# Kernel optimization log

Measured on AMD Instinct MI355X. Metric: run time of the kernel, lower is better.

The kernel has to match this reference:

```python
import jax, jax.numpy as jnp
import numpy as np

P_SCALAR = 40.0
NEG_INF = -1e9


def setup_inputs() -> dict:
    key = jax.random.key(0)
    ks = jax.random.split(key, 6)
    B, Dk, Dv, T, H, W = 2, 128, 512, 2, 64, 64
    qkey = jax.random.normal(ks[0], (B, Dk, H, W), dtype=jnp.float32)
    qval = jax.random.normal(ks[1], (B, Dv, H, W), dtype=jnp.float32)
    mkey = jax.random.normal(ks[2], (B, Dk, T, H, W), dtype=jnp.float32)
    mval = jax.random.normal(ks[3], (B, Dv, T, H, W), dtype=jnp.float32)
    qmask = jax.random.bernoulli(ks[4], 0.5, (B, 1, H, W))
    mmask = jax.random.bernoulli(ks[5], 0.5, (B, 1, T, H, W))
    return {"qkey": qkey, "qval": qval, "qmask": qmask,
            "mkey": mkey, "mval": mval, "mmask": mmask}


def reference(qkey, qval, qmask, mkey, mval, mmask):
    # Faithful vectorized version of maskRead: for each batch, attention from
    # masked query pixels over masked memory pixels, scatter back into zeros.
    # Boolean-gather + softmax over gathered rows == full softmax with masked
    # logits set to -inf (rows outside mmask get zero probability).
    B, Dk, H, W = qkey.shape
    Dv = qval.shape[1]
    qk = qkey.reshape(B, Dk, H * W)            # [B, Dk, Nq]
    mk = mkey.reshape(B, Dk, -1)               # [B, Dk, Nm]
    mv = mval.reshape(B, Dv, -1)               # [B, Dv, Nm]
    qm = qmask.reshape(B, H * W)               # [B, Nq]
    mm = mmask.reshape(B, -1)                  # [B, Nm]

    # p[b, m, q] = <mk[b,:,m], qk[b,:,q]> * p_scalar, softmax over m
    p = jnp.einsum('bdm,bdq->bmq', mk, qk) * P_SCALAR
    p = jnp.where(mm[:, :, None], p, NEG_INF)
    p = jax.nn.softmax(p, axis=1)              # [B, Nm, Nq]

    read = jnp.einsum('bvm,bmq->bvq', mv, p)   # [B, Dv, Nq]

    # zero out query pixels outside qmask; skip batches with empty masks
    valid = qm[:, None, :] & mm.any(axis=1)[:, None, None] & qm.any(axis=1)[:, None, None]
    qread = jnp.where(valid, read, 0.0)
    return qread.reshape(B, Dv, H, W)
```

## Files before the change

### kernel.cpp

```cpp
#include <hip/hip_runtime.h>

#define NQ 4096
#define NM 8192
#define DK 128
#define DV 512
#define BATCH 2
#define NT (NM / 64)
#define KTS 8192
#define VTILE 16384

typedef __attribute__((ext_vector_type(8))) short short8;
typedef __attribute__((ext_vector_type(4))) float f32x4;
typedef unsigned short ushort_t;

#define MF(A_, B_, C_) __builtin_amdgcn_mfma_f32_16x16x32_bf16(A_, B_, C_, 0, 0, 0)

static __device__ __forceinline__ unsigned short f2bf(float x) {
    union { float f; unsigned int u; } c; c.f = x;
    unsigned int u = c.u;
    return (unsigned short)((u + 0x7FFFu + ((u >> 16) & 1u)) >> 16);
}
static __device__ __forceinline__ float bf2f(unsigned short h) {
    union { unsigned int u; float f; } c; c.u = ((unsigned int)h) << 16;
    return c.f;
}

static __device__ __forceinline__ size_t vaddr(int b, int pos, int dv) {
    const int mt = pos >> 6, m64 = pos & 63;
    const int dvh = dv >> 8, rr = dv & 255;
    return (((size_t)(b * NT + mt) * 2 + dvh) * VTILE)
         + (rr >> 6) * 4096 + ((rr >> 4) & 3) * 1024
         + (m64 >> 5) * 512
         + ((((m64 >> 4) & 1) * 2 + ((m64 >> 3) & 1)) * 128)
         + (rr & 15) * 8 + (m64 & 7);
}

#define LOADK(AH, AL, itn_) do {                                              \
    const size_t ktb_ = kbase + (size_t)(itn_) * KTS;                         \
    _Pragma("unroll")                                                         \
    for (int ks_ = 0; ks_ < 4; ++ks_) {                                       \
        AH[ks_] = *(const short8*)(kh0 + ktb_ + ks_ * 512);                   \
        AL[ks_] = *(const short8*)(kl0 + ktb_ + ks_ * 512);                   \
    }                                                                         \
} while (0)

__global__ __launch_bounds__(1024) void scan_kernel(
    const int* __restrict__ qmask, const int* __restrict__ mmask,
    int* __restrict__ cidx, int* __restrict__ cpos,
    int* __restrict__ cnts, int* __restrict__ qflags) {
    const int b = blockIdx.x;
    const int t = threadIdx.x;
    const int lane = t & 63;
    const int w = t >> 6;
    __shared__ int wsum[16];
    __shared__ int qsh;

    const int* mp = mmask + b * NM;
    const int base = t * 8;
    int val[8];
#pragma unroll
    for (int i = 0; i < 8; ++i) val[i] = (mp[base + i] != 0);
    int c0 = 0;
#pragma unroll
    for (int i = 0; i < 8; ++i) c0 += val[i];

    int c = c0;
#pragma unroll
    for (int off = 1; off < 64; off <<= 1) {
        int n = __shfl_up(c, off, 64);
        if (lane >= off) c += n;
    }
    if (lane == 63) wsum[w] = c;
    if (t == 0) qsh = 0;
    __syncthreads();
    if (t == 0) {
        int s = 0;
#pragma unroll
        for (int i = 0; i < 16; ++i) { s += wsum[i]; wsum[i] = s; }
    }
    __syncthreads();
    const int wbase = (w == 0) ? 0 : wsum[w - 1];
    int run = wbase + (c - c0);
#pragma unroll
    for (int i = 0; i < 8; ++i) {
        int m = base + i;
        cpos[b * NM + m] = run;
        if (val[i]) { cidx[b * NM + run] = m; ++run; }
    }

    int qa = 0;
    for (int i = t; i < NQ; i += 1024) qa |= (qmask[b * NQ + i] != 0);
    if (qa) atomicOr(&qsh, 1);
    __syncthreads();
    if (t == 0) { cnts[b] = wsum[15]; qflags[b] = qsh; }
}

__global__ __launch_bounds__(256) void prep_q_kernel(
    const float* __restrict__ src, ushort_t* __restrict__ hi,
    ushort_t* __restrict__ lo) {
    const int b = blockIdx.z;
    const int d0 = blockIdx.y * 32;
    const int n0 = blockIdx.x * 32;
    __shared__ float t32[32][33];
    for (int l = threadIdx.x; l < 1024; l += 256) {
        int r = l >> 5, c = l & 31;
        t32[r][c] = src[((size_t)b * DK + d0 + r) * NQ + n0 + c];
    }
    __syncthreads();
    for (int l = threadIdx.x; l < 1024; l += 256) {
        int r = l >> 5, c = l & 31;
        float f = t32[c][r];
        unsigned short h = f2bf(f);
        unsigned short lw = f2bf(f - bf2f(h));
        size_t off = ((size_t)b * NQ + n0 + r) * DK + d0 + c;
        hi[off] = h;
        lo[off] = lw;
    }
}

__global__ __launch_bounds__(256) void prep_k_kernel(
    const float* __restrict__ src, const int* __restrict__ mmask,
    const int* __restrict__ cpos,
    ushort_t* __restrict__ hi, ushort_t* __restrict__ lo) {
    const int b = blockIdx.z;
    const int d0 = blockIdx.y * 32;
    const int n0 = blockIdx.x * 32;
    __shared__ float t32[32][33];
    for (int l = threadIdx.x; l < 1024; l += 256) {
        int r = l >> 5, c = l & 31;
        t32[r][c] = src[((size_t)b * DK + d0 + r) * NM + n0 + c];
    }
    __syncthreads();
    for (int l = threadIdx.x; l < 1024; l += 256) {
        int r = l >> 5, c = l & 31;
        int m = n0 + r;
        if (mmask[b * NM + m] != 0) {
            int pos = cpos[b * NM + m];
            float f = t32[c][r];
            unsigned short h = f2bf(f);
            unsigned short lw = f2bf(f - bf2f(h));
            int d = d0 + c;
            size_t off = ((size_t)(b * NT + (pos >> 6))) * KTS
                       + ((pos >> 4) & 3) * 2048 + (d >> 5) * 512
                       + ((d >> 3) & 3) * 128 + (pos & 15) * 8 + (d & 7);
            hi[off] = h;
            lo[off] = lw;
        }
    }
}

__global__ __launch_bounds__(256) void prep_v_kernel(
    const float* __restrict__ src, const int* __restrict__ mmask,
    const int* __restrict__ cpos, const int* __restrict__ cnts,
    ushort_t* __restrict__ dst) {
    const int b = blockIdx.z;
    const int dv0 = blockIdx.x * 8;
    if (blockIdx.y == 8) {
        const int cnt = cnts[b];
        const int pend = ((cnt + 63) >> 6) * 64;
        const int dv = dv0 + (threadIdx.x >> 5);
        for (int p = cnt + (threadIdx.x & 31); p < pend; p += 32)
            dst[vaddr(b, p, dv)] = 0;
        return;
    }
    const int m = blockIdx.y * 1024 + threadIdx.x * 4;
    const int4 mm = *(const int4*)(mmask + b * NM + m);
    const int4 cp = *(const int4*)(cpos + b * NM + m);
#pragma unroll
    for (int i = 0; i < 8; ++i) {
        const int dv = dv0 + i;
        const float4 v = *(const float4*)(src + ((size_t)b * DV + dv) * NM + m);
        if (mm.x) dst[vaddr(b, cp.x, dv)] = f2bf(v.x);
        if (mm.y) dst[vaddr(b, cp.y, dv)] = f2bf(v.y);
        if (mm.z) dst[vaddr(b, cp.z, dv)] = f2bf(v.z);
        if (mm.w) dst[vaddr(b, cp.w, dv)] = f2bf(v.w);
    }
}

__global__ __launch_bounds__(256, 4) void stats_kernel(
    const ushort_t* __restrict__ Qhi, const ushort_t* __restrict__ Khi,
    const int* __restrict__ cnts, float* __restrict__ mpart) {
    const int t = threadIdx.x;
    const int lane = t & 63;
    const int w = t >> 6;
    const int quad = lane >> 4;
    const int col = lane & 15;
    const int bid = blockIdx.x;
    const int part = bid & 3;
    const int b = (bid >> 2) & 1;
    const int qb = (bid >> 3) * 32;

    const int cnt = cnts[b];
    const int nit = (cnt + 63) >> 6;
    const int it0 = (nit * part) >> 2;
    const int it1 = (nit * (part + 1)) >> 2;

    __shared__ float red_m[4][32];

    short8 qfh[2][4];
    {
        const ushort_t* qhp = Qhi + ((size_t)b * NQ + qb) * DK;
#pragma unroll
        for (int qt = 0; qt < 2; ++qt)
#pragma unroll
            for (int ks = 0; ks < 4; ++ks)
                qfh[qt][ks] = *(const short8*)(qhp + (size_t)(qt * 16 + col) * DK + ks * 32 + quad * 8);
    }

    const f32x4 zero4 = {0.f, 0.f, 0.f, 0.f};
    float mloc[2] = {-3.0e38f, -3.0e38f};
    const ushort_t* kh0 = Khi + w * 2048 + lane * 8;
    const size_t kbase = (size_t)(b * NT) * KTS;

#define LOADKH(A_, itn_) do {                                                 \
    const size_t ktb_ = kbase + (size_t)(itn_) * KTS;                         \
    _Pragma("unroll")                                                         \
    for (int ks_ = 0; ks_ < 4; ++ks_)                                         \
        A_[ks_] = *(const short8*)(kh0 + ktb_ + ks_ * 512);                   \
} while (0)

#define STPH(CK, NK, it_, itn_) do {                                          \
    LOADKH(NK, itn_);                                                         \
    f32x4 aS0 = zero4, aS1 = zero4;                                           \
    _Pragma("unroll")                                                         \
    for (int ks = 0; ks < 4; ++ks) {                                          \
        aS0 = MF(CK[ks], qfh[0][ks], aS0);                                    \
        aS1 = MF(CK[ks], qfh[1][ks], aS1);                                    \
    }                                                                         \
    const int mrow_ = (it_) * 64 + w * 16 + quad * 4;                         \
    _Pragma("unroll")                                                         \
    for (int r = 0; r < 4; ++r) {                                             \
        if (mrow_ + r < cnt) {                                                \
            mloc[0] = fmaxf(mloc[0], aS0[r] * 40.0f);                         \
            mloc[1] = fmaxf(mloc[1], aS1[r] * 40.0f);                         \
        }                                                                     \
    }                                                                         \
} while (0)

    short8 kA[4], kB[4];
    int it = it0;
    if (it < it1) {
        LOADKH(kA, it);
        int itn;
        while (true) {
            itn = (it + 1 < it1) ? it + 1 : it;
            STPH(kA, kB, it, itn);
            if (++it >= it1) break;
            itn = (it + 1 < it1) ? it + 1 : it;
            STPH(kB, kA, it, itn);
            if (++it >= it1) break;
        }
    }
#undef STPH
#undef LOADKH

#pragma unroll
    for (int qt = 0; qt < 2; ++qt) {
        float m = mloc[qt];
        m = fmaxf(m, __shfl_xor(m, 16, 64));
        m = fmaxf(m, __shfl_xor(m, 32, 64));
        if (lane < 16) red_m[w][qt * 16 + col] = m;
    }
    __syncthreads();
    if (t < 32) {
        float M = -3.0e38f;
#pragma unroll
        for (int ww = 0; ww < 4; ++ww) M = fmaxf(M, red_m[ww][t]);
        mpart[((size_t)(b * 4 + part)) * NQ + qb + t] = M;
    }
}

__global__ __launch_bounds__(256, 2) void pv_kernel(
    const ushort_t* __restrict__ Qhi, const ushort_t* __restrict__ Qlo,
    const ushort_t* __restrict__ Khi, const ushort_t* __restrict__ Klo,
    const ushort_t* __restrict__ Vimg, const int* __restrict__ cnts,
    const int* __restrict__ qflags, const int* __restrict__ qmask,
    const float* __restrict__ mpart, float* __restrict__ out) {
    const int t = threadIdx.x;
    const int lane = t & 63;
    const int w = t >> 6;
    const int quad = lane >> 4;
    const int col = lane & 15;
    const int bid = blockIdx.x;
    const int cmb = bid & 3;
    const int b = cmb >> 1;
    const int dvh = cmb & 1;
    const int qb = (bid >> 2) * 32;

    const int cnt = cnts[b];
    const int it1 = (cnt + 63) >> 6;

    __shared__ __align__(16) ushort_t P_s[2][32][68];
    __shared__ float l_s[32];

    float gm0, gm1;
    {
        float M0 = -3.0e38f, M1 = -3.0e38f;
#pragma unroll
        for (int c = 0; c < 4; ++c) {
            M0 = fmaxf(M0, mpart[((size_t)(b * 4 + c)) * NQ + qb + col]);
            M1 = fmaxf(M1, mpart[((size_t)(b * 4 + c)) * NQ + qb + 16 + col]);
        }
        gm0 = M0 + 8.0f;
        gm1 = M1 + 8.0f;
    }

    short8 qfh[2][4], qfl[2][4];
    {
        const ushort_t* qhp = Qhi + ((size_t)b * NQ + qb) * DK;
        const ushort_t* qlp = Qlo + ((size_t)b * NQ + qb) * DK;
#pragma unroll
        for (int qt = 0; qt < 2; ++qt)
#pragma unroll
            for (int ks = 0; ks < 4; ++ks) {
                size_t off = (size_t)(qt * 16 + col) * DK + ks * 32 + quad * 8;
                qfh[qt][ks] = *(const short8*)(qhp + off);
                qfl[qt][ks] = *(const short8*)(qlp + off);
            }
    }

    const ushort_t* kh0 = Khi + w * 2048 + lane * 8;
    const ushort_t* kl0 = Klo + w * 2048 + lane * 8;
    const size_t kbase = (size_t)(b * NT) * KTS;
    const ushort_t* vl0 = Vimg + ((size_t)(b * NT) * 2 + dvh) * VTILE
                        + w * 4096 + lane * 8;

    const f32x4 zero4 = {0.f, 0.f, 0.f, 0.f};
    const short8 vones = {(short)0x3F80, (short)0x3F80, (short)0x3F80,
                          (short)0x3F80, (short)0x3F80, (short)0x3F80,
                          (short)0x3F80, (short)0x3F80};
    const bool doL = (w == 0);
    f32x4 accO[4][2];
#pragma unroll
    for (int vt = 0; vt < 4; ++vt)
#pragma unroll
        for (int qt = 0; qt < 2; ++qt) accO[vt][qt] = zero4;
    f32x4 accL0 = zero4, accL1 = zero4;

#define PV_PHASE(CKH, CKL, NKH, NKL, PB, it_, itn_) do {                      \
    const ushort_t* vp_ = vl0 + (size_t)(it_) * (2 * VTILE);                  \
    short8 vf_[4][2];                                                         \
    _Pragma("unroll")                                                         \
    for (int vt = 0; vt < 4; ++vt) {                                          \
        vf_[vt][0] = *(const short8*)(vp_ + vt * 1024);                       \
        vf_[vt][1] = *(const short8*)(vp_ + vt * 1024 + 512);                 \
    }                                                                         \
    f32x4 aS0 = zero4, aS1 = zero4;                                           \
    _Pragma("unroll")                                                         \
    for (int ks = 0; ks < 4; ++ks) {                                          \
        aS0 = MF(CKH[ks], qfh[0][ks], aS0); aS1 = MF(CKH[ks], qfh[1][ks], aS1); \
        aS0 = MF(CKH[ks], qfl[0][ks], aS0); aS1 = MF(CKH[ks], qfl[1][ks], aS1); \
        aS0 = MF(CKL[ks], qfh[0][ks], aS0); aS1 = MF(CKL[ks], qfh[1][ks], aS1); \
    }                                                                         \
    LOADK(NKH, NKL, itn_);                                                    \
    const int mrow_ = (it_) * 64 + w * 16 + quad * 4;                         \
    {                                                                         \
        float p_[4]; ushort4 pk_;                                             \
        _Pragma("unroll")                                                     \
        for (int r = 0; r < 4; ++r)                                           \
            p_[r] = (mrow_ + r < cnt) ? __expf(aS0[r] * 40.0f - gm0) : 0.0f;  \
        pk_.x = f2bf(p_[0]); pk_.y = f2bf(p_[1]);                             \
        pk_.z = f2bf(p_[2]); pk_.w = f2bf(p_[3]);                             \
        *(ushort4*)&P_s[PB][col][w * 16 + quad * 4] = pk_;                    \
        _Pragma("unroll")                                                     \
        for (int r = 0; r < 4; ++r)                                           \
            p_[r] = (mrow_ + r < cnt) ? __expf(aS1[r] * 40.0f - gm1) : 0.0f;  \
        pk_.x = f2bf(p_[0]); pk_.y = f2bf(p_[1]);                             \
        pk_.z = f2bf(p_[2]); pk_.w = f2bf(p_[3]);                             \
        *(ushort4*)&P_s[PB][16 + col][w * 16 + quad * 4] = pk_;               \
    }                                                                         \
    asm volatile("s_waitcnt lgkmcnt(0)" ::: "memory");                        \
    __builtin_amdgcn_s_barrier();                                             \
    __builtin_amdgcn_sched_barrier(0);                                        \
    _Pragma("unroll")                                                         \
    for (int k2 = 0; k2 < 2; ++k2) {                                          \
        short8 pb0_ = *(const short8*)&P_s[PB][col][k2 * 32 + quad * 8];      \
        short8 pb1_ = *(const short8*)&P_s[PB][16 + col][k2 * 32 + quad * 8]; \
        _Pragma("unroll")                                                     \
        for (int vt = 0; vt < 4; ++vt) {                                      \
            accO[vt][0] = MF(vf_[vt][k2], pb0_, accO[vt][0]);                 \
            accO[vt][1] = MF(vf_[vt][k2], pb1_, accO[vt][1]);                 \
        }                                                                     \
        if (doL) {                                                            \
            accL0 = MF(vones, pb0_, accL0);                                   \
            accL1 = MF(vones, pb1_, accL1);                                   \
        }                                                                     \
    }                                                                         \
} while (0)

    short8 kAh[4], kAl[4], kBh[4], kBl[4];
    int it = 0;
    if (it < it1) {
        LOADK(kAh, kAl, it);
        int itn;
        while (true) {
            itn = (it + 1 < it1) ? it + 1 : it;
            PV_PHASE(kAh, kAl, kBh, kBl, 0, it, itn);
            if (++it >= it1) break;
            itn = (it + 1 < it1) ? it + 1 : it;
            PV_PHASE(kBh, kBl, kAh, kAl, 1, it, itn);
            if (++it >= it1) break;
        }
    }
#undef PV_PHASE

    if (doL && lane < 16) {
        l_s[col] = accL0[0];
        l_s[16 + col] = accL1[0];
    }
    __syncthreads();
    const int qflag = qflags[b];
#pragma unroll
    for (int qt = 0; qt < 2; ++qt) {
        const int q = qb + qt * 16 + col;
        const float L = l_s[qt * 16 + col];
        const bool valid = (qflag != 0) && (cnt > 0) &&
                           (qmask[b * NQ + q] != 0) && (L > 0.f);
        const float rinv = valid ? 1.0f / L : 0.0f;
#pragma unroll
        for (int vt = 0; vt < 4; ++vt)
#pragma unroll
            for (int r = 0; r < 4; ++r) {
                int dv = dvh * 256 + w * 64 + vt * 16 + quad * 4 + r;
                out[((size_t)b * DV + dv) * NQ + q] = accO[vt][qt][r] * rinv;
            }
    }
}

extern "C" void kernel_launch(void* const* d_in, const int* in_sizes, int n_in,
                              void* d_out, int out_size, void* d_ws, size_t ws_size,
                              hipStream_t stream) {
    const float* qkey  = (const float*)d_in[0];
    const int*   qmask = (const int*)d_in[2];
    const float* mkey  = (const float*)d_in[3];
    const float* mval  = (const float*)d_in[4];
    const int*   mmask = (const int*)d_in[5];
    float* out = (float*)d_out;

    char* ws = (char*)d_ws;
    size_t off = 0;
    const size_t QS  = (size_t)BATCH * NQ * DK * 2;
    const size_t KS2 = (size_t)BATCH * NM * DK * 2;
    const size_t VS  = (size_t)BATCH * NT * 2 * VTILE * 2;
    ushort_t* Qhi = (ushort_t*)(ws + off); off += QS;
    ushort_t* Qlo = (ushort_t*)(ws + off); off += QS;
    ushort_t* Khi = (ushort_t*)(ws + off); off += KS2;
    ushort_t* Klo = (ushort_t*)(ws + off); off += KS2;
    ushort_t* Vc  = (ushort_t*)(ws + off); off += VS;
    float* mpart  = (float*)(ws + off); off += (size_t)BATCH * 4 * NQ * 4;
    int* cidx     = (int*)(ws + off); off += (size_t)BATCH * NM * 4;
    int* cpos     = (int*)(ws + off); off += (size_t)BATCH * NM * 4;
    int* cnts     = (int*)(ws + off); off += 64;
    int* qflags   = (int*)(ws + off); off += 64;

    scan_kernel<<<BATCH, 1024, 0, stream>>>(qmask, mmask, cidx, cpos, cnts, qflags);

    dim3 gq(NQ / 32, DK / 32, BATCH);
    prep_q_kernel<<<gq, 256, 0, stream>>>(qkey, Qhi, Qlo);
    dim3 gk(NM / 32, DK / 32, BATCH);
    prep_k_kernel<<<gk, 256, 0, stream>>>(mkey, mmask, cpos, Khi, Klo);

    dim3 gv(DV / 8, 9, BATCH);
    prep_v_kernel<<<gv, 256, 0, stream>>>(mval, mmask, cpos, cnts, Vc);

    stats_kernel<<<(NQ / 32) * 8, 256, 0, stream>>>(Qhi, Khi, cnts, mpart);

    pv_kernel<<<(NQ / 32) * 4, 256, 0, stream>>>(
        Qhi, Qlo, Khi, Klo, Vc, cnts, qflags, qmask, mpart, out);
}
```

Measured before the change: 234.8 us.

## Split PV over memory chunks with 64-query tiles and a combine pass

The PV kernel now handles 64 queries per block instead of 32, with Q fragments staged in shared memory, and splits the memory (key) loop into two halves run by separate blocks. Each half writes unnormalized partial outputs and row sums, and a new combine kernel adds the halves, normalizes and applies the masks. The larger query tile reuses each K/V load across more queries, and the split restores the block count to keep parallelism. In exchange the code writes and reads an extra full-size output buffer, adds a launch, and drops the explicit double-buffered K register prefetch.

```diff
diff --git a/kernel.cpp b/kernel.cpp
--- a/kernel.cpp
+++ b/kernel.cpp
@@ -274,50 +274,50 @@
     const ushort_t* __restrict__ Qhi, const ushort_t* __restrict__ Qlo,
     const ushort_t* __restrict__ Khi, const ushort_t* __restrict__ Klo,
     const ushort_t* __restrict__ Vimg, const int* __restrict__ cnts,
-    const int* __restrict__ qflags, const int* __restrict__ qmask,
-    const float* __restrict__ mpart, float* __restrict__ out) {
+    const float* __restrict__ mpart, float* __restrict__ out0,
+    float* __restrict__ out1, float* __restrict__ lsum) {
     const int t = threadIdx.x;
     const int lane = t & 63;
     const int w = t >> 6;
     const int quad = lane >> 4;
     const int col = lane & 15;
     const int bid = blockIdx.x;
-    const int cmb = bid & 3;
-    const int b = cmb >> 1;
-    const int dvh = cmb & 1;
-    const int qb = (bid >> 2) * 32;
+    const int chunk = bid & 1;
+    const int dvh = (bid >> 1) & 1;
+    const int b = (bid >> 2) & 1;
+    const int qb = (bid >> 3) * 64;
 
     const int cnt = cnts[b];
-    const int it1 = (cnt + 63) >> 6;
-
-    __shared__ __align__(16) ushort_t P_s[2][32][68];
-    __shared__ float l_s[32];
-
-    float gm0, gm1;
+    const int nit = (cnt + 63) >> 6;
+    const int nh = (nit + 1) >> 1;
+    const int it0 = chunk ? nh : 0;
+    const int it1 = chunk ? nit : nh;
+
+    __shared__ __align__(16) ushort_t Q_s[2][4][4][512];
+    __shared__ __align__(16) ushort_t P_s[2][64][68];
+
+    float gm[4];
+#pragma unroll
+    for (int qt = 0; qt < 4; ++qt) {
+        float M = -3.0e38f;
+#pragma unroll
+        for (int c = 0; c < 4; ++c)
+            M = fmaxf(M, mpart[((size_t)(b * 4 + c)) * NQ + qb + qt * 16 + col]);
+        gm[qt] = M + 8.0f;
+    }
+
     {
-        float M0 = -3.0e38f, M1 = -3.0e38f;
-#pragma unroll
-        for (int c = 0; c < 4; ++c) {
-            M0 = fmaxf(M0, mpart[((size_t)(b * 4 + c)) * NQ + qb + col]);
-            M1 = fmaxf(M1, mpart[((size_t)(b * 4 + c)) * NQ + qb + 16 + col]);
-        }
-        gm0 = M0 + 8.0f;
-        gm1 = M1 + 8.0f;
-    }
-
-    short8 qfh[2][4], qfl[2][4];
-    {
-        const ushort_t* qhp = Qhi + ((size_t)b * NQ + qb) * DK;
-        const ushort_t* qlp = Qlo + ((size_t)b * NQ + qb) * DK;
-#pragma unroll
-        for (int qt = 0; qt < 2; ++qt)
-#pragma unroll
-            for (int ks = 0; ks < 4; ++ks) {
-                size_t off = (size_t)(qt * 16 + col) * DK + ks * 32 + quad * 8;
-                qfh[qt][ks] = *(const short8*)(qhp + off);
-                qfl[qt][ks] = *(const short8*)(qlp + off);
-            }
-    }
+        const int r = t >> 2, ks4 = t & 3;
+        const int qt_ = r >> 4, col_ = r & 15;
+        const ushort_t* qhp = Qhi + ((size_t)b * NQ + qb + r) * DK + ks4 * 32;
+        const ushort_t* qlp = Qlo + ((size_t)b * NQ + qb + r) * DK + ks4 * 32;
+#pragma unroll
+        for (int qd = 0; qd < 4; ++qd) {
+            *(short8*)&Q_s[0][qt_][ks4][qd * 128 + col_ * 8] = *(const short8*)(qhp + qd * 8);
+            *(short8*)&Q_s[1][qt_][ks4][qd * 128 + col_ * 8] = *(const short8*)(qlp + qd * 8);
+        }
+    }
+    __syncthreads();
 
     const ushort_t* kh0 = Khi + w * 2048 + lane * 8;
     const ushort_t* kl0 = Klo + w * 2048 + lane * 8;
@@ -329,102 +329,115 @@
     const short8 vones = {(short)0x3F80, (short)0x3F80, (short)0x3F80,
                           (short)0x3F80, (short)0x3F80, (short)0x3F80,
                           (short)0x3F80, (short)0x3F80};
-    const bool doL = (w == 0);
-    f32x4 accO[4][2];
+    const bool doL = (dvh == 0) && (w == 0);
+    f32x4 accO[4][4];
 #pragma unroll
     for (int vt = 0; vt < 4; ++vt)
 #pragma unroll
-        for (int qt = 0; qt < 2; ++qt) accO[vt][qt] = zero4;
-    f32x4 accL0 = zero4, accL1 = zero4;
-
-#define PV_PHASE(CKH, CKL, NKH, NKL, PB, it_, itn_) do {                      \
-    const ushort_t* vp_ = vl0 + (size_t)(it_) * (2 * VTILE);                  \
-    short8 vf_[4][2];                                                         \
-    _Pragma("unroll")                                                         \
-    for (int vt = 0; vt < 4; ++vt) {                                          \
-        vf_[vt][0] = *(const short8*)(vp_ + vt * 1024);                       \
-        vf_[vt][1] = *(const short8*)(vp_ + vt * 1024 + 512);                 \
-    }                                                                         \
-    f32x4 aS0 = zero4, aS1 = zero4;                                           \
-    _Pragma("unroll")                                                         \
-    for (int ks = 0; ks < 4; ++ks) {                                          \
-        aS0 = MF(CKH[ks], qfh[0][ks], aS0); aS1 = MF(CKH[ks], qfh[1][ks], aS1); \
-        aS0 = MF(CKH[ks], qfl[0][ks], aS0); aS1 = MF(CKH[ks], qfl[1][ks], aS1); \
-        aS0 = MF(CKL[ks], qfh[0][ks], aS0); aS1 = MF(CKL[ks], qfh[1][ks], aS1); \
-    }                                                                         \
-    LOADK(NKH, NKL, itn_);                                                    \
-    const int mrow_ = (it_) * 64 + w * 16 + quad * 4;                         \
-    {                                                                         \
-        float p_[4]; ushort4 pk_;                                             \
-        _Pragma("unroll")                                                     \
-        for (int r = 0; r < 4; ++r)                                           \
-            p_[r] = (mrow_ + r < cnt) ? __expf(aS0[r] * 40.0f - gm0) : 0.0f;  \
-        pk_.x = f2bf(p_[0]); pk_.y = f2bf(p_[1]);                             \
-        pk_.z = f2bf(p_[2]); pk_.w = f2bf(p_[3]);                             \
-        *(ushort4*)&P_s[PB][col][w * 16 + quad * 4] = pk_;                    \
-        _Pragma("unroll")                                                     \
-        for (int r = 0; r < 4; ++r)                                           \
-            p_[r] = (mrow_ + r < cnt) ? __expf(aS1[r] * 40.0f - gm1) : 0.0f;  \
-        pk_.x = f2bf(p_[0]); pk_.y = f2bf(p_[1]);                             \
-        pk_.z = f2bf(p_[2]); pk_.w = f2bf(p_[3]);                             \
-        *(ushort4*)&P_s[PB][16 + col][w * 16 + quad * 4] = pk_;               \
-    }                                                                         \
-    asm volatile("s_waitcnt lgkmcnt(0)" ::: "memory");                        \
-    __builtin_amdgcn_s_barrier();                                             \
-    __builtin_amdgcn_sched_barrier(0);                                        \
-    _Pragma("unroll")                                                         \
-    for (int k2 = 0; k2 < 2; ++k2) {                                          \
-        short8 pb0_ = *(const short8*)&P_s[PB][col][k2 * 32 + quad * 8];      \
-        short8 pb1_ = *(const short8*)&P_s[PB][16 + col][k2 * 32 + quad * 8]; \
-        _Pragma("unroll")                                                     \
-        for (int vt = 0; vt < 4; ++vt) {                                      \
-            accO[vt][0] = MF(vf_[vt][k2], pb0_, accO[vt][0]);                 \
-            accO[vt][1] = MF(vf_[vt][k2], pb1_, accO[vt][1]);                 \
-        }                                                                     \
-        if (doL) {                                                            \
-            accL0 = MF(vones, pb0_, accL0);                                   \
-            accL1 = MF(vones, pb1_, accL1);                                   \
-        }                                                                     \
-    }                                                                         \
-} while (0)
-
-    short8 kAh[4], kAl[4], kBh[4], kBl[4];
-    int it = 0;
-    if (it < it1) {
-        LOADK(kAh, kAl, it);
-        int itn;
-        while (true) {
-            itn = (it + 1 < it1) ? it + 1 : it;
-            PV_PHASE(kAh, kAl, kBh, kBl, 0, it, itn);
-            if (++it >= it1) break;
-            itn = (it + 1 < it1) ? it + 1 : it;
-            PV_PHASE(kBh, kBl, kAh, kAl, 1, it, itn);
-            if (++it >= it1) break;
-        }
-    }
-#undef PV_PHASE
-
-    if (doL && lane < 16) {
-        l_s[col] = accL0[0];
-        l_s[16 + col] = accL1[0];
-    }
-    __syncthreads();
-    const int qflag = qflags[b];
-#pragma unroll
-    for (int qt = 0; qt < 2; ++qt) {
+        for (int qt = 0; qt < 4; ++qt) accO[vt][qt] = zero4;
+    f32x4 accL[4];
+#pragma unroll
+    for (int qt = 0; qt < 4; ++qt) accL[qt] = zero4;
+
+    for (int it = it0; it < it1; ++it) {
+        const int pb = (it - it0) & 1;
+        short8 kh[4], kl[4];
+        LOADK(kh, kl, it);
+        f32x4 aS[4];
+#pragma unroll
+        for (int qt = 0; qt < 4; ++qt) aS[qt] = zero4;
+#pragma unroll
+        for (int qt = 0; qt < 4; ++qt) {
+#pragma unroll
+            for (int ks = 0; ks < 4; ++ks) {
+                const short8 qh = *(const short8*)&Q_s[0][qt][ks][lane * 8];
+                const short8 ql = *(const short8*)&Q_s[1][qt][ks][lane * 8];
+                aS[qt] = MF(kh[ks], qh, aS[qt]);
+                aS[qt] = MF(kh[ks], ql, aS[qt]);
+                aS[qt] = MF(kl[ks], qh, aS[qt]);
+            }
+        }
+        const ushort_t* vp = vl0 + (size_t)it * (2 * VTILE);
+        short8 vf[4][2];
+#pragma unroll
+        for (int vt = 0; vt < 4; ++vt) {
+            vf[vt][0] = *(const short8*)(vp + vt * 1024);
+            vf[vt][1] = *(const short8*)(vp + vt * 1024 + 512);
+        }
+        const int mrow = it * 64 + w * 16 + quad * 4;
+#pragma unroll
+        for (int qt = 0; qt < 4; ++qt) {
+            float p[4];
+#pragma unroll
+            for (int r = 0; r < 4; ++r)
+                p[r] = (mrow + r < cnt) ? __expf(aS[qt][r] * 40.0f - gm[qt]) : 0.0f;
+            ushort4 pk;
+            pk.x = f2bf(p[0]); pk.y = f2bf(p[1]);
+            pk.z = f2bf(p[2]); pk.w = f2bf(p[3]);
+            *(ushort4*)&P_s[pb][qt * 16 + col][w * 16 + quad * 4] = pk;
+        }
+        asm volatile("s_waitcnt lgkmcnt(0)" ::: "memory");
+        __builtin_amdgcn_s_barrier();
+        __builtin_amdgcn_sched_barrier(0);
+#pragma unroll
+        for (int k2 = 0; k2 < 2; ++k2) {
+            short8 pq[4];
+#pragma unroll
+            for (int qt = 0; qt < 4; ++qt)
+                pq[qt] = *(const short8*)&P_s[pb][qt * 16 + col][k2 * 32 + quad * 8];
+#pragma unroll
+            for (int vt = 0; vt < 4; ++vt)
+#pragma unroll
+                for (int qt = 0; qt < 4; ++qt)
+                    accO[vt][qt] = MF(vf[vt][k2], pq[qt], accO[vt][qt]);
+            if (doL) {
+#pragma unroll
+                for (int qt = 0; qt < 4; ++qt)
+                    accL[qt] = MF(vones, pq[qt], accL[qt]);
+            }
+        }
+    }
+
+    float* pbase = chunk ? out1 : out0;
+#pragma unroll
+    for (int qt = 0; qt < 4; ++qt) {
         const int q = qb + qt * 16 + col;
-        const float L = l_s[qt * 16 + col];
-        const bool valid = (qflag != 0) && (cnt > 0) &&
-                           (qmask[b * NQ + q] != 0) && (L > 0.f);
-        const float rinv = valid ? 1.0f / L : 0.0f;
 #pragma unroll
         for (int vt = 0; vt < 4; ++vt)
 #pragma unroll
             for (int r = 0; r < 4; ++r) {
                 int dv = dvh * 256 + w * 64 + vt * 16 + quad * 4 + r;
-                out[((size_t)b * DV + dv) * NQ + q] = accO[vt][qt][r] * rinv;
+                pbase[((size_t)b * DV + dv) * NQ + q] = accO[vt][qt][r];
             }
     }
+    if (doL && lane < 16) {
+#pragma unroll
+        for (int qt = 0; qt < 4; ++qt)
+            lsum[((size_t)(b * 2 + chunk)) * NQ + qb + qt * 16 + col] = accL[qt][0];
+    }
+}
+
+__global__ __launch_bounds__(256) void combine_kernel(
+    const float* p0, const float* __restrict__ p1,
+    const float* __restrict__ lsum, const int* __restrict__ cnts,
+    const int* __restrict__ qflags, const int* __restrict__ qmask,
+    float* out) {
+    const size_t i = ((size_t)blockIdx.x * 256 + threadIdx.x) * 4;
+    const int b = (int)(i >> 21);
+    const int q = (int)(i & (NQ - 1));
+    f32x4 a = *(const f32x4*)(p0 + i);
+    f32x4 c = *(const f32x4*)(p1 + i);
+    f32x4 l0 = *(const f32x4*)(lsum + (size_t)(b * 2) * NQ + q);
+    f32x4 l1 = *(const f32x4*)(lsum + (size_t)(b * 2 + 1) * NQ + q);
+    const int4 qm = *(const int4*)(qmask + b * NQ + q);
+    const bool bv = (qflags[b] != 0) && (cnts[b] > 0);
+    f32x4 r;
+    float lv;
+    lv = l0[0] + l1[0]; r[0] = (bv && qm.x && lv > 0.f) ? (a[0] + c[0]) / lv : 0.f;
+    lv = l0[1] + l1[1]; r[1] = (bv && qm.y && lv > 0.f) ? (a[1] + c[1]) / lv : 0.f;
+    lv = l0[2] + l1[2]; r[2] = (bv && qm.z && lv > 0.f) ? (a[2] + c[2]) / lv : 0.f;
+    lv = l0[3] + l1[3]; r[3] = (bv && qm.w && lv > 0.f) ? (a[3] + c[3]) / lv : 0.f;
+    *(f32x4*)(out + i) = r;
 }
 
 extern "C" void kernel_launch(void* const* d_in, const int* in_sizes, int n_in,
@@ -442,12 +455,15 @@
     const size_t QS  = (size_t)BATCH * NQ * DK * 2;
     const size_t KS2 = (size_t)BATCH * NM * DK * 2;
     const size_t VS  = (size_t)BATCH * NT * 2 * VTILE * 2;
+    const size_t OS  = (size_t)BATCH * DV * NQ * 4;
     ushort_t* Qhi = (ushort_t*)(ws + off); off += QS;
     ushort_t* Qlo = (ushort_t*)(ws + off); off += QS;
     ushort_t* Khi = (ushort_t*)(ws + off); off += KS2;
     ushort_t* Klo = (ushort_t*)(ws + off); off += KS2;
     ushort_t* Vc  = (ushort_t*)(ws + off); off += VS;
+    float* part1  = (float*)(ws + off); off += OS;
     float* mpart  = (float*)(ws + off); off += (size_t)BATCH * 4 * NQ * 4;
+    float* lsum   = (float*)(ws + off); off += (size_t)BATCH * 2 * NQ * 4;
     int* cidx     = (int*)(ws + off); off += (size_t)BATCH * NM * 4;
     int* cpos     = (int*)(ws + off); off += (size_t)BATCH * NM * 4;
     int* cnts     = (int*)(ws + off); off += 64;
@@ -465,6 +481,9 @@
 
     stats_kernel<<<(NQ / 32) * 8, 256, 0, stream>>>(Qhi, Khi, cnts, mpart);
 
-    pv_kernel<<<(NQ / 32) * 4, 256, 0, stream>>>(
-        Qhi, Qlo, Khi, Klo, Vc, cnts, qflags, qmask, mpart, out);
-}
+    pv_kernel<<<(NQ / 64) * 8, 256, 0, stream>>>(
+        Qhi, Qlo, Khi, Klo, Vc, cnts, mpart, out, part1, lsum);
+
+    combine_kernel<<<(int)((size_t)BATCH * DV * NQ / 1024), 256, 0, stream>>>(
+        out, part1, lsum, cnts, qflags, qmask, out);
+}
```

New measurement: 237.4 us. No clear change (+1.1%).
